# Kernel tuning notes

Hardware: AMD Instinct MI355X
Metric: run time of the kernel (lower is better)

Reference implementation:

```python
import jax, jax.numpy as jnp
import numpy as np

B, D, U = 8192, 128, 128  # batch, input_dim, units (D == U required by the tile/reshape sign path)
CLIP = 20.0
EPS = 1e-7


def setup_inputs() -> dict:
    key = jax.random.key(0)
    ks = jax.random.split(key, 6)
    x = jax.random.normal(ks[0], (B, D), dtype=jnp.float32)
    # initializers: w ~ N(1, 0.1), m ~ N(-1, 0.1), g ~ N(0, 0.1)
    w_hat = 1.0 + 0.1 * jax.random.normal(ks[1], (D, U), dtype=jnp.float32)
    m_hat = -1.0 + 0.1 * jax.random.normal(ks[2], (D, U), dtype=jnp.float32)
    w_hat_prime = 1.0 + 0.1 * jax.random.normal(ks[3], (D, U), dtype=jnp.float32)
    m_hat_prime = -1.0 + 0.1 * jax.random.normal(ks[4], (D, U), dtype=jnp.float32)
    g = 0.1 * jax.random.normal(ks[5], (U,), dtype=jnp.float32)
    return {"x": x, "w_hat": w_hat, "m_hat": m_hat,
            "w_hat_prime": w_hat_prime, "m_hat_prime": m_hat_prime, "g": g}


def reference(x, w_hat, m_hat, w_hat_prime, m_hat_prime, g):
    w1 = jnp.tanh(w_hat) * jax.nn.sigmoid(m_hat)            # [D, U]
    w2 = jnp.tanh(w_hat_prime) * jax.nn.sigmoid(m_hat_prime)  # [D, U]
    a1 = x @ w1                                              # additive path [B, U]
    # multiplicative (log-space) path
    m1 = jnp.exp(jnp.minimum(jnp.log(jnp.maximum(jnp.abs(x), EPS)) @ w2, CLIP))
    # sign-correction path: faithful to tf concat/reshape layout
    w1s = jnp.abs(w2).reshape(-1)                            # [D*U], row-major over (D, U)
    xs = jnp.tile(x, (1, U))                                 # [B, U*D]
    sgn = jnp.sign(xs) * w1s + (1.0 - w1s)                   # [B, D*U]
    ms = jnp.prod(sgn.reshape(-1, U, D), axis=2)             # [B, U]
    g1 = jax.nn.sigmoid(g)                                   # [U]
    return g1 * a1 + (1.0 - g1) * m1 * jnp.clip(ms, -1.0, 1.0)
```

## Files before the change

kernel.cpp:

```cpp
#include <hip/hip_runtime.h>
#include <cmath>


typedef __bf16  bf16x8 __attribute__((ext_vector_type(8)));
typedef float   f32x4  __attribute__((ext_vector_type(4)));

#define NROWS 8192
#define KDIM  128
#define UDIM  128

__device__ __forceinline__ unsigned short f2bf(float f) {
    union { float f; unsigned int u; } v; v.f = f;
    unsigned int u = v.u;
    unsigned int r = (u + 0x7FFFu + ((u >> 16) & 1u)) >> 16;
    return (unsigned short)r;
}

__device__ __forceinline__ unsigned int pck(unsigned short a, unsigned short b) {
    return (unsigned int)a | ((unsigned int)b << 16);
}

__device__ __forceinline__ float sigmoidf_(float v) {
    return 1.0f / (1.0f + expf(-v));
}

__global__ void nalu_prep(const float* __restrict__ w_hat,
                          const float* __restrict__ m_hat,
                          const float* __restrict__ whp,
                          const float* __restrict__ mhp,
                          unsigned short* __restrict__ Bsw) {
    int i = blockIdx.x * 256 + threadIdx.x;
    int n = i >> 7;
    int k = i & 127;
    int dk = k * 128 + n;
    int ud = n * 128 + k;

    float w1v = tanhf(w_hat[dk]) * sigmoidf_(m_hat[dk]);
    float w2v = tanhf(whp[dk])   * sigmoidf_(mhp[dk]);
    float a   = fabsf(tanhf(whp[ud]) * sigmoidf_(mhp[ud]));
    float f   = 1.0f - 2.0f * a;
    float Sv  = fmaxf(logf(fmaxf(fabsf(f), 1e-38f)), -80.0f);
    float ngv = (f < 0.0f) ? 1.0f : 0.0f;

    int nblk = n >> 4, l16 = n & 15, kstep = k >> 5, quad = (k >> 3) & 3, j = k & 7;
    int lane = quad * 16 + l16;
    int base = ((nblk * 4 + kstep) * 64 + lane) * 8 + j;
    const int MATSTRIDE = 8 * 4 * 64 * 8;

    Bsw[base]                 = f2bf(w1v);
    Bsw[base + MATSTRIDE]     = f2bf(w2v);
    Bsw[base + 2 * MATSTRIDE] = f2bf(Sv);
    Bsw[base + 3 * MATSTRIDE] = f2bf(ngv);
}

__global__ __launch_bounds__(256, 1)
void nalu_main(const float* __restrict__ x,
               const unsigned short* __restrict__ Bsw,
               const float* __restrict__ g,
               float* __restrict__ out) {
    __shared__ __align__(16) unsigned short As[3][32][136];

    const int t    = threadIdx.x;
    const int wave = t >> 6;
    const int lane = t & 63;
    const int quad = lane >> 4;
    const int l16  = lane & 15;
    const int rowblk = blockIdx.x * 32;

    bf16x8 Bf[4][2][4];
    const bf16x8* Bp = reinterpret_cast<const bf16x8*>(Bsw);
    #pragma unroll
    for (int mat = 0; mat < 4; ++mat)
        #pragma unroll
        for (int ns = 0; ns < 2; ++ns)
            #pragma unroll
            for (int ks = 0; ks < 4; ++ks) {
                int nblk = wave * 2 + ns;
                Bf[mat][ns][ks] = Bp[((mat * 8 + nblk) * 4 + ks) * 64 + lane];
            }

    const float4* xv = reinterpret_cast<const float4*>(x + rowblk * 128);
    #pragma unroll
    for (int it = 0; it < 4; ++it) {
        int idx  = t + it * 256;
        int row  = idx >> 5;
        int col4 = idx & 31;
        float4 v = xv[idx];
        float vv[4] = {v.x, v.y, v.z, v.w};
        unsigned short sx[4], sl[4], sn[4];
        #pragma unroll
        for (int j = 0; j < 4; ++j) {
            float f = vv[j];
            sx[j] = f2bf(f);
            sl[j] = f2bf(logf(fmaxf(fabsf(f), 1e-7f)));
            sn[j] = (f < 0.0f) ? 0x3F80u : 0u;
        }
        uint2 px = {pck(sx[0], sx[1]), pck(sx[2], sx[3])};
        uint2 pl = {pck(sl[0], sl[1]), pck(sl[2], sl[3])};
        uint2 pn = {pck(sn[0], sn[1]), pck(sn[2], sn[3])};
        *reinterpret_cast<uint2*>(&As[0][row][col4 * 4]) = px;
        *reinterpret_cast<uint2*>(&As[1][row][col4 * 4]) = pl;
        *reinterpret_cast<uint2*>(&As[2][row][col4 * 4]) = pn;
    }
    __syncthreads();

    f32x4 accA[2][2], accM[2][2], accS[2][2], accC[2][2];
    #pragma unroll
    for (int ms = 0; ms < 2; ++ms)
        #pragma unroll
        for (int ns = 0; ns < 2; ++ns) {
            f32x4 z = {0.0f, 0.0f, 0.0f, 0.0f};
            accA[ms][ns] = z; accM[ms][ns] = z; accS[ms][ns] = z; accC[ms][ns] = z;
        }

    #pragma unroll
    for (int ks = 0; ks < 4; ++ks) {
        bf16x8 Ax[2], Al[2], An[2];
        #pragma unroll
        for (int ms = 0; ms < 2; ++ms) {
            int m = ms * 16 + l16;
            int k = ks * 32 + quad * 8;
            Ax[ms] = *reinterpret_cast<const bf16x8*>(&As[0][m][k]);
            Al[ms] = *reinterpret_cast<const bf16x8*>(&As[1][m][k]);
            An[ms] = *reinterpret_cast<const bf16x8*>(&As[2][m][k]);
        }
        #pragma unroll
        for (int ms = 0; ms < 2; ++ms)
            #pragma unroll
            for (int ns = 0; ns < 2; ++ns) {
                accA[ms][ns] = __builtin_amdgcn_mfma_f32_16x16x32_bf16(Ax[ms], Bf[0][ns][ks], accA[ms][ns], 0, 0, 0);
                accM[ms][ns] = __builtin_amdgcn_mfma_f32_16x16x32_bf16(Al[ms], Bf[1][ns][ks], accM[ms][ns], 0, 0, 0);
                accS[ms][ns] = __builtin_amdgcn_mfma_f32_16x16x32_bf16(An[ms], Bf[2][ns][ks], accS[ms][ns], 0, 0, 0);
                accC[ms][ns] = __builtin_amdgcn_mfma_f32_16x16x32_bf16(An[ms], Bf[3][ns][ks], accC[ms][ns], 0, 0, 0);
            }
    }

    #pragma unroll
    for (int ns = 0; ns < 2; ++ns) {
        int u = wave * 32 + ns * 16 + l16;
        float g1 = sigmoidf_(g[u]);
        float om = 1.0f - g1;
        #pragma unroll
        for (int ms = 0; ms < 2; ++ms) {
            int rbase = rowblk + ms * 16 + quad * 4;
            #pragma unroll
            for (int r = 0; r < 4; ++r) {
                float a1 = accA[ms][ns][r];
                float ml = accM[ms][ns][r];
                float sl = accS[ms][ns][r];
                float cn = accC[ms][ns][r];
                float par = 1.0f - 2.0f * (cn - 2.0f * floorf(cn * 0.5f));
                float mterm = par * expf(fminf(ml, 20.0f) + sl);
                out[(rbase + r) * 128 + u] = g1 * a1 + om * mterm;
            }
        }
    }
}

extern "C" void kernel_launch(void* const* d_in, const int* in_sizes, int n_in,
                              void* d_out, int out_size, void* d_ws, size_t ws_size,
                              hipStream_t stream) {
    const float* x     = (const float*)d_in[0];
    const float* w_hat = (const float*)d_in[1];
    const float* m_hat = (const float*)d_in[2];
    const float* whp   = (const float*)d_in[3];
    const float* mhp   = (const float*)d_in[4];
    const float* g     = (const float*)d_in[5];
    unsigned short* Bsw = (unsigned short*)d_ws;
    float* outp = (float*)d_out;

    nalu_prep<<<64, 256, 0, stream>>>(w_hat, m_hat, whp, mhp, Bsw);
    nalu_main<<<256, 256, 0, stream>>>(x, Bsw, g, outp);
}
```

Measured before the change: 71.78 us.

## Fuse weight prep into main kernel via cooperative grid sync and fast math

Merges the separate weight-preparation kernel into the main kernel. Each block computes a 64-element slice of the transformed weight fragments, writes them to workspace, converts its x tile into LDS, then does a grid-wide cooperative sync before loading the weights. This removes the second launch and the dependency gap between the kernels. It also switches tanh, sigmoid, log and exp to fast intrinsics, which may reduce accuracy, and adds the cost of a grid barrier across 256 blocks.

Result: slower. 121.1 us (+68.7%).

```diff
diff --git a/kernel.cpp b/kernel.cpp
--- a/kernel.cpp
+++ b/kernel.cpp
@@ -1,13 +1,12 @@
 #include <hip/hip_runtime.h>
+#include <hip/hip_cooperative_groups.h>
 #include <cmath>
+
+namespace cg = cooperative_groups;
 
 
 typedef __bf16  bf16x8 __attribute__((ext_vector_type(8)));
 typedef float   f32x4  __attribute__((ext_vector_type(4)));
-
-#define NROWS 8192
-#define KDIM  128
-#define UDIM  128
 
 __device__ __forceinline__ unsigned short f2bf(float f) {
     union { float f; unsigned int u; } v; v.f = f;
@@ -20,44 +19,27 @@
     return (unsigned int)a | ((unsigned int)b << 16);
 }
 
-__device__ __forceinline__ float sigmoidf_(float v) {
-    return 1.0f / (1.0f + expf(-v));
+__device__ __forceinline__ float fast_sig(float v) {
+    return 1.0f / (1.0f + __expf(-v));
+}
+__device__ __forceinline__ float fast_tanh(float v) {
+    return 1.0f - 2.0f / (1.0f + __expf(2.0f * v));
 }
 
-__global__ void nalu_prep(const float* __restrict__ w_hat,
-                          const float* __restrict__ m_hat,
-                          const float* __restrict__ whp,
-                          const float* __restrict__ mhp,
-                          unsigned short* __restrict__ Bsw) {
-    int i = blockIdx.x * 256 + threadIdx.x;
-    int n = i >> 7;
-    int k = i & 127;
-    int dk = k * 128 + n;
-    int ud = n * 128 + k;
-
-    float w1v = tanhf(w_hat[dk]) * sigmoidf_(m_hat[dk]);
-    float w2v = tanhf(whp[dk])   * sigmoidf_(mhp[dk]);
-    float a   = fabsf(tanhf(whp[ud]) * sigmoidf_(mhp[ud]));
-    float f   = 1.0f - 2.0f * a;
-    float Sv  = fmaxf(logf(fmaxf(fabsf(f), 1e-38f)), -80.0f);
-    float ngv = (f < 0.0f) ? 1.0f : 0.0f;
-
+__device__ __forceinline__ int fragaddr(int n, int k) {
     int nblk = n >> 4, l16 = n & 15, kstep = k >> 5, quad = (k >> 3) & 3, j = k & 7;
-    int lane = quad * 16 + l16;
-    int base = ((nblk * 4 + kstep) * 64 + lane) * 8 + j;
-    const int MATSTRIDE = 8 * 4 * 64 * 8;
-
-    Bsw[base]                 = f2bf(w1v);
-    Bsw[base + MATSTRIDE]     = f2bf(w2v);
-    Bsw[base + 2 * MATSTRIDE] = f2bf(Sv);
-    Bsw[base + 3 * MATSTRIDE] = f2bf(ngv);
+    return (((nblk * 4 + kstep) * 64 + quad * 16 + l16) * 8) + j;
 }
 
 __global__ __launch_bounds__(256, 1)
-void nalu_main(const float* __restrict__ x,
-               const unsigned short* __restrict__ Bsw,
-               const float* __restrict__ g,
-               float* __restrict__ out) {
+void nalu_fused(const float* __restrict__ x,
+                const float* __restrict__ w_hat,
+                const float* __restrict__ m_hat,
+                const float* __restrict__ whp,
+                const float* __restrict__ mhp,
+                const float* __restrict__ g,
+                unsigned short* __restrict__ Bsw,
+                float* __restrict__ out) {
     __shared__ __align__(16) unsigned short As[3][32][136];
 
     const int t    = threadIdx.x;
@@ -66,6 +48,58 @@
     const int quad = lane >> 4;
     const int l16  = lane & 15;
     const int rowblk = blockIdx.x * 32;
+
+    const float4* xv = reinterpret_cast<const float4*>(x + rowblk * 128);
+    float4 vbuf[4];
+    #pragma unroll
+    for (int it = 0; it < 4; ++it) vbuf[it] = xv[t + it * 256];
+
+    if (t < 64) {
+        int e  = blockIdx.x * 64 + t;
+        int d  = e >> 7;
+        int u  = e & 127;
+        int dk = d * 128 + u;
+
+        float w1v = fast_tanh(w_hat[dk]) * fast_sig(m_hat[dk]);
+        float w2v = fast_tanh(whp[dk])   * fast_sig(mhp[dk]);
+        float a   = fabsf(w2v);
+        float f   = 1.0f - 2.0f * a;
+        float Sv  = fmaxf(__logf(fmaxf(fabsf(f), 1e-38f)), -80.0f);
+        float ngv = (f < 0.0f) ? 1.0f : 0.0f;
+
+        const int MS = 16384;
+        Bsw[fragaddr(u, d)]          = f2bf(w1v);
+        Bsw[fragaddr(u, d) + MS]     = f2bf(w2v);
+        Bsw[fragaddr(d, u) + 2 * MS] = f2bf(Sv);
+        Bsw[fragaddr(d, u) + 3 * MS] = f2bf(ngv);
+    }
+
+    #pragma unroll
+    for (int it = 0; it < 4; ++it) {
+        int idx  = t + it * 256;
+        int row  = idx >> 5;
+        int col4 = idx & 31;
+        float4 v = vbuf[it];
+        float vv[4] = {v.x, v.y, v.z, v.w};
+        unsigned short sx[4], sl[4], sn[4];
+        #pragma unroll
+        for (int j = 0; j < 4; ++j) {
+            float f = vv[j];
+            sx[j] = f2bf(f);
+            sl[j] = f2bf(__logf(fmaxf(fabsf(f), 1e-7f)));
+            sn[j] = (f < 0.0f) ? 0x3F80u : 0u;
+        }
+        uint2 px = {pck(sx[0], sx[1]), pck(sx[2], sx[3])};
+        uint2 pl = {pck(sl[0], sl[1]), pck(sl[2], sl[3])};
+        uint2 pn = {pck(sn[0], sn[1]), pck(sn[2], sn[3])};
+        *reinterpret_cast<uint2*>(&As[0][row][col4 * 4]) = px;
+        *reinterpret_cast<uint2*>(&As[1][row][col4 * 4]) = pl;
+        *reinterpret_cast<uint2*>(&As[2][row][col4 * 4]) = pn;
+    }
+    __syncthreads();
+
+    __threadfence();
+    cg::this_grid().sync();
 
     bf16x8 Bf[4][2][4];
     const bf16x8* Bp = reinterpret_cast<const bf16x8*>(Bsw);
@@ -78,31 +112,6 @@
                 int nblk = wave * 2 + ns;
                 Bf[mat][ns][ks] = Bp[((mat * 8 + nblk) * 4 + ks) * 64 + lane];
             }
-
-    const float4* xv = reinterpret_cast<const float4*>(x + rowblk * 128);
-    #pragma unroll
-    for (int it = 0; it < 4; ++it) {
-        int idx  = t + it * 256;
-        int row  = idx >> 5;
-        int col4 = idx & 31;
-        float4 v = xv[idx];
-        float vv[4] = {v.x, v.y, v.z, v.w};
-        unsigned short sx[4], sl[4], sn[4];
-        #pragma unroll
-        for (int j = 0; j < 4; ++j) {
-            float f = vv[j];
-            sx[j] = f2bf(f);
-            sl[j] = f2bf(logf(fmaxf(fabsf(f), 1e-7f)));
-            sn[j] = (f < 0.0f) ? 0x3F80u : 0u;
-        }
-        uint2 px = {pck(sx[0], sx[1]), pck(sx[2], sx[3])};
-        uint2 pl = {pck(sl[0], sl[1]), pck(sl[2], sl[3])};
-        uint2 pn = {pck(sn[0], sn[1]), pck(sn[2], sn[3])};
-        *reinterpret_cast<uint2*>(&As[0][row][col4 * 4]) = px;
-        *reinterpret_cast<uint2*>(&As[1][row][col4 * 4]) = pl;
-        *reinterpret_cast<uint2*>(&As[2][row][col4 * 4]) = pn;
-    }
-    __syncthreads();
 
     f32x4 accA[2][2], accM[2][2], accS[2][2], accC[2][2];
     #pragma unroll
@@ -138,7 +147,7 @@
     #pragma unroll
     for (int ns = 0; ns < 2; ++ns) {
         int u = wave * 32 + ns * 16 + l16;
-        float g1 = sigmoidf_(g[u]);
+        float g1 = fast_sig(g[u]);
         float om = 1.0f - g1;
         #pragma unroll
         for (int ms = 0; ms < 2; ++ms) {
@@ -150,7 +159,7 @@
                 float sl = accS[ms][ns][r];
                 float cn = accC[ms][ns][r];
                 float par = 1.0f - 2.0f * (cn - 2.0f * floorf(cn * 0.5f));
-                float mterm = par * expf(fminf(ml, 20.0f) + sl);
+                float mterm = par * __expf(fminf(ml, 20.0f) + sl);
                 out[(rbase + r) * 128 + u] = g1 * a1 + om * mterm;
             }
         }
@@ -169,6 +178,8 @@
     unsigned short* Bsw = (unsigned short*)d_ws;
     float* outp = (float*)d_out;
 
-    nalu_prep<<<64, 256, 0, stream>>>(w_hat, m_hat, whp, mhp, Bsw);
-    nalu_main<<<256, 256, 0, stream>>>(x, Bsw, g, outp);
+    void* args[] = {(void*)&x, (void*)&w_hat, (void*)&m_hat, (void*)&whp,
+                    (void*)&mhp, (void*)&g, (void*)&Bsw, (void*)&outp};
+    hipLaunchCooperativeKernel((const void*)nalu_fused, dim3(256), dim3(256),
+                               args, 0, stream);
 }
```
